# Kernel optimization log

Measured on AMD Instinct MI355X. Metric: run time of the kernel, lower is better.

Reference implementation:

```python
import jax, jax.numpy as jnp
import numpy as np

N_NODES = 50000
N_EDGES = 800000
IN_DIM = 256
HID = 64
HEADS = 4
OUT_DIM = 16
N_GRAPHS = 64
NEG_SLOPE = 0.2


def setup_inputs() -> dict:
    key = jax.random.key(0)
    ks = jax.random.split(key, 16)
    H2 = HID // 2  # conv2 out channels (heads=1, concat=False)
    H4 = HID // 4
    inp = {
        "x": jax.random.normal(ks[0], (N_NODES, IN_DIM), jnp.float32),
        "edge_index": jax.random.randint(ks[1], (2, N_EDGES), 0, N_NODES, jnp.int64),
        "batch": jnp.sort(jax.random.randint(ks[2], (N_NODES,), 0, N_GRAPHS, jnp.int64)),
        # GATConv 1: in=IN_DIM, out=HID, heads=HEADS, concat=True
        "W1": jax.random.normal(ks[3], (IN_DIM, HEADS * HID), jnp.float32) * 0.05,
        "att_src1": jax.random.normal(ks[4], (HEADS, HID), jnp.float32) * 0.1,
        "att_dst1": jax.random.normal(ks[5], (HEADS, HID), jnp.float32) * 0.1,
        "b1": jnp.zeros((HEADS * HID,), jnp.float32),
        # GATConv 2: in=HEADS*HID, out=HID/2, heads=1, concat=False
        "W2": jax.random.normal(ks[6], (HEADS * HID, H2), jnp.float32) * 0.05,
        "att_src2": jax.random.normal(ks[7], (1, H2), jnp.float32) * 0.1,
        "att_dst2": jax.random.normal(ks[8], (1, H2), jnp.float32) * 0.1,
        "b2": jnp.zeros((H2,), jnp.float32),
        "fc1_w": jax.random.normal(ks[9], (H2, H4), jnp.float32) * 0.1,
        "fc1_b": jnp.zeros((H4,), jnp.float32),
        "fc2_w": jax.random.normal(ks[10], (H4, OUT_DIM), jnp.float32) * 0.1,
        "fc2_b": jnp.zeros((OUT_DIM,), jnp.float32),
    }
    return inp


def gat_conv(x, W, att_src, att_dst, bias, src, dst, num_nodes, concat):
    """PyG-style GATConv (eval mode, self-loops already in src/dst)."""
    H, C = att_src.shape
    h = (x @ W).reshape(num_nodes, H, C)          # [N,H,C]
    a_src = (h * att_src).sum(-1)                 # [N,H]
    a_dst = (h * att_dst).sum(-1)                 # [N,H]
    e = jax.nn.leaky_relu(a_src[src] + a_dst[dst], NEG_SLOPE)  # [E,H]
    # segment softmax over destination nodes (self-loops => every segment nonempty)
    emax = jax.ops.segment_max(e, dst, num_segments=num_nodes)
    ex = jnp.exp(e - emax[dst])
    denom = jax.ops.segment_sum(ex, dst, num_segments=num_nodes)
    alpha = ex / (denom[dst] + 1e-16)             # [E,H]
    msg = h[src] * alpha[:, :, None]              # [E,H,C]
    out = jax.ops.segment_sum(msg, dst, num_segments=num_nodes)  # [N,H,C]
    out = out.reshape(num_nodes, H * C) if concat else out.mean(axis=1)
    return out + bias


def reference(x, edge_index, batch, W1, att_src1, att_dst1, b1,
              W2, att_src2, att_dst2, b2, fc1_w, fc1_b, fc2_w, fc2_b):
    num_nodes = x.shape[0]
    loops = jnp.arange(num_nodes, dtype=edge_index.dtype)
    src = jnp.concatenate([edge_index[0], loops])
    dst = jnp.concatenate([edge_index[1], loops])

    h = gat_conv(x, W1, att_src1, att_dst1, b1, src, dst, num_nodes, concat=True)
    h = jax.nn.relu(h)                                 # dropout: eval no-op
    h = gat_conv(h, W2, att_src2, att_dst2, b2, src, dst, num_nodes, concat=False)

    # global mean pool over graphs
    sums = jax.ops.segment_sum(h, batch, num_segments=N_GRAPHS)
    cnts = jax.ops.segment_sum(jnp.ones((num_nodes,), h.dtype), batch, num_segments=N_GRAPHS)
    g = sums / jnp.maximum(cnts, 1.0)[:, None]         # [G, HID/2]

    g = jax.nn.relu(g)
    g = jax.nn.relu(g @ fc1_w + fc1_b)
    g = jax.nn.relu(g @ fc2_w + fc2_b)
    return g
```

## Files before the change

kernel.cpp:

```cpp
#include <hip/hip_runtime.h>
#include <math.h>

#define NEG 0.2f
#define LMAX 1024
#define CAP 1600
#define SCHUNK 2048
typedef unsigned short u16;
typedef unsigned int u32;
typedef __bf16 bf16x8 __attribute__((ext_vector_type(8)));
typedef float f32x4 __attribute__((ext_vector_type(4)));

__device__ __forceinline__ float bf2f(u16 u) {
    union { unsigned i; float f; } x; x.i = ((unsigned)u) << 16; return x.f;
}
__device__ __forceinline__ u16 f2bf(float f) {
    union { float f; unsigned u; } x; x.f = f;
    unsigned r = x.u + 0x7fffu + ((x.u >> 16) & 1u);
    return (u16)(r >> 16);
}

__global__ void prep_all(const float* __restrict__ W1, const float* __restrict__ att_s1,
                         const float* __restrict__ att_d1, u16* __restrict__ w1x,
                         const float* __restrict__ W2, const float* __restrict__ att_s2,
                         const float* __restrict__ att_d2, u16* __restrict__ w2x,
                         int* __restrict__ bktcur, int NBK) {
    int t = threadIdx.x;
    if (blockIdx.x < 256) {
        int k = blockIdx.x;
        int c = t;
        float w = W1[k * 256 + c];
        w1x[c * 256 + k] = f2bf(w);
        int head = c >> 6;
        float vs = w * att_s1[c];
        float vd = w * att_d1[c];
#pragma unroll
        for (int mask = 1; mask < 64; mask <<= 1) {
            vs += __shfl_xor(vs, mask, 64);
            vd += __shfl_xor(vd, mask, 64);
        }
        if ((c & 63) == 0) {
            w1x[(256 + head) * 256 + k] = f2bf(vs);
            w1x[(260 + head) * 256 + k] = f2bf(vd);
            w1x[(264 + head) * 256 + k] = 0;
            w1x[(268 + head) * 256 + k] = 0;
        }
    } else {
        int k = t;
        float a_s = 0.f, a_d = 0.f;
#pragma unroll
        for (int j = 0; j < 32; ++j) {
            float w = W2[k * 32 + j];
            w2x[j * 256 + k] = f2bf(w);
            a_s += w * att_s2[j];
            a_d += w * att_d2[j];
        }
        w2x[32 * 256 + k] = f2bf(a_s);
        w2x[33 * 256 + k] = f2bf(a_d);
#pragma unroll
        for (int r = 34; r < 48; ++r) w2x[r * 256 + k] = 0;
        for (int i = t; i < NBK; i += 256) bktcur[i] = 0;
    }
}

__global__ __launch_bounds__(512) void gemm1_and_scatter(
        const float* __restrict__ x, const u16* __restrict__ w1x,
        u16* __restrict__ h1b, float* __restrict__ asad, int N,
        const int* __restrict__ ei, int* __restrict__ bktcur,
        u32* __restrict__ ebuf, int E, int ET, int NBK) {
    __shared__ __align__(16) u16 xs[2][16][264];
    __shared__ int lcnt[LMAX];
    __shared__ int lbase[LMAX];
    int t = threadIdx.x;

    if (blockIdx.x < 256) {
        int wave = t >> 6, lane = t & 63;
        int g = lane >> 4, l15 = lane & 15;

        bf16x8 wreg[3][8];
#pragma unroll
        for (int ci = 0; ci < 3; ++ci) {
            int ct = (ci == 2) ? 16 : (wave * 2 + ci);
            const u16* wp = w1x + (size_t)(ct * 16 + l15) * 256 + g * 8;
#pragma unroll
            for (int ks = 0; ks < 8; ++ks)
                wreg[ci][ks] = *reinterpret_cast<const bf16x8*>(wp + ks * 32);
        }

        int srow = t >> 5, sseg = t & 31;
        int ntiles = (N + 15) >> 4;
        int tile0 = blockIdx.x;
        if (tile0 >= ntiles) return;

        auto stage_load = [&](int tile, float4& a0, float4& a1) {
            int arow = tile * 16 + srow; if (arow > N - 1) arow = N - 1;
            const float* xp = x + (size_t)arow * 256 + sseg * 8;
            a0 = *reinterpret_cast<const float4*>(xp);
            a1 = *reinterpret_cast<const float4*>(xp + 4);
        };
        auto stage_write = [&](int buf, const float4& a0, const float4& a1) {
            uint4 o;
            o.x = (unsigned)f2bf(a0.x) | ((unsigned)f2bf(a0.y) << 16);
            o.y = (unsigned)f2bf(a0.z) | ((unsigned)f2bf(a0.w) << 16);
            o.z = (unsigned)f2bf(a1.x) | ((unsigned)f2bf(a1.y) << 16);
            o.w = (unsigned)f2bf(a1.z) | ((unsigned)f2bf(a1.w) << 16);
            *reinterpret_cast<uint4*>(&xs[buf][srow][sseg * 8]) = o;
        };

        {
            float4 a0, a1;
            stage_load(tile0, a0, a1);
            stage_write(0, a0, a1);
        }
        __syncthreads();

        int cur = 0;
        for (int tile = tile0; tile < ntiles; tile += 256) {
            int nxt = tile + 256;
            bool hasnext = nxt < ntiles;
            float4 p0, p1;
            if (hasnext) stage_load(nxt, p0, p1);

            f32x4 acc[3];
#pragma unroll
            for (int ci = 0; ci < 3; ++ci) acc[ci] = (f32x4){0.f, 0.f, 0.f, 0.f};
#pragma unroll
            for (int ks = 0; ks < 8; ++ks) {
                bf16x8 bfr = *reinterpret_cast<const bf16x8*>(&xs[cur][l15][ks * 32 + g * 8]);
#pragma unroll
                for (int ci = 0; ci < 3; ++ci)
                    acc[ci] = __builtin_amdgcn_mfma_f32_16x16x32_bf16(wreg[ci][ks], bfr, acc[ci], 0, 0, 0);
            }

            int nrow = tile * 16 + l15;
            if (nrow < N) {
#pragma unroll
                for (int ci = 0; ci < 2; ++ci) {
                    int ct = wave * 2 + ci;
                    ushort4 o;
                    o.x = f2bf(acc[ci][0]); o.y = f2bf(acc[ci][1]);
                    o.z = f2bf(acc[ci][2]); o.w = f2bf(acc[ci][3]);
                    *reinterpret_cast<ushort4*>(h1b + (size_t)nrow * 256 + ct * 16 + g * 4) = o;
                }
                if (wave == 0 && g < 2) {
#pragma unroll
                    for (int reg = 0; reg < 4; ++reg)
                        asad[(size_t)nrow * 8 + g * 4 + reg] = acc[2][reg];
                }
            }
            __syncthreads();
            if (hasnext) stage_write(cur ^ 1, p0, p1);
            __syncthreads();
            cur ^= 1;
        }
    } else {
        int cb = blockIdx.x - 256;
        for (int b = t; b < NBK; b += 512) lcnt[b] = 0;
        __syncthreads();
        int base = cb * SCHUNK;
#pragma unroll
        for (int k = 0; k < SCHUNK / 512; ++k) {
            int i = base + k * 512 + t;
            if (i < ET) {
                int d = (i < E) ? ei[E + i] : (i - E);
                atomicAdd(&lcnt[d >> 6], 1);
            }
        }
        __syncthreads();
        for (int b = t; b < NBK; b += 512) {
            int c = lcnt[b];
            lbase[b] = c ? (b * CAP + atomicAdd(&bktcur[b], c)) : 0;
        }
        __syncthreads();
        for (int b = t; b < NBK; b += 512) lcnt[b] = 0;
        __syncthreads();
#pragma unroll
        for (int k = 0; k < SCHUNK / 512; ++k) {
            int i = base + k * 512 + t;
            if (i < ET) {
                int s, d;
                if (i < E) { s = ei[i]; d = ei[E + i]; }
                else       { s = i - E; d = s; }
                int b = d >> 6;
                int idx = atomicAdd(&lcnt[b], 1);
                ebuf[lbase[b] + idx] = (u32)s | ((u32)(d & 63) << 16);
            }
        }
    }
}

__global__ __launch_bounds__(256) void bucket_csr_pad(const u32* __restrict__ ebuf,
                                                      const int* __restrict__ bktcur,
                                                      int* __restrict__ row_ptr,
                                                      int* __restrict__ rowend,
                                                      int* __restrict__ col, int N) {
    __shared__ int cnt[64];
    __shared__ int cur[64];
    int b = blockIdx.x, t = threadIdx.x;
    int v0 = b << 6;
    int s0 = b * CAP, s1 = s0 + bktcur[b];
    if (t < 64) cnt[t] = 0;
    __syncthreads();
    for (int i = s0 + t; i < s1; i += 256)
        atomicAdd(&cnt[(ebuf[i] >> 16) & 63], 1);
    __syncthreads();
    if (t < 64) {
        int c = cnt[t];
        int val = c;
#pragma unroll
        for (int off = 1; off < 64; off <<= 1) {
            int n = __shfl_up(val, off, 64);
            if (t >= off) val += n;
        }
        int excl = s0 + val - c;
        if (v0 + t < N) { row_ptr[v0 + t] = excl; rowend[v0 + t] = excl + c; }
        cur[t] = excl;
    }
    __syncthreads();
    for (int i = s0 + t; i < s1; i += 256) {
        u32 v = ebuf[i];
        int pos = atomicAdd(&cur[(v >> 16) & 63], 1);
        col[pos] = (int)(v & 0xFFFFu);
    }
}

__global__ __launch_bounds__(256) void conv1_fused(const u16* __restrict__ h1b,
                                                   const float* __restrict__ asad,
                                                   const int* __restrict__ row_ptr,
                                                   const int* __restrict__ rowend,
                                                   const int* __restrict__ col,
                                                   const float* __restrict__ b1,
                                                   u16* __restrict__ hin2b, int N) {
    __shared__ float la[4][128][4];
    __shared__ int   lc[4][128];
    int idx = blockIdx.x * blockDim.x + threadIdx.x;
    int v = idx >> 6; if (v > N - 1) v = N - 1;
    int lane = idx & 63;
    int node = threadIdx.x >> 6;
    int head = lane >> 4, l15 = lane & 15;
    float adst = asad[(size_t)v * 8 + 4 + head];
    int beg = row_ptr[v], end = rowend[v];
    int deg = end - beg;
    bool fast = (deg <= 128);
    float m = -1e30f, l = 0.f;
    if (fast) {
        float e[8]; int u[8];
#pragma unroll
        for (int i = 0; i < 8; ++i) {
            int p = beg + l15 + i * 16;
            float ev = -1e30f; int uu = 0;
            if (p < end) {
                uu = col[p];
                float tv = asad[(size_t)uu * 8 + head] + adst;
                ev = tv > 0.f ? tv : NEG * tv;
            }
            e[i] = ev; u[i] = uu;
        }
        m = e[0];
#pragma unroll
        for (int i = 1; i < 8; ++i) m = fmaxf(m, e[i]);
#pragma unroll
        for (int mask = 1; mask < 16; mask <<= 1) m = fmaxf(m, __shfl_xor(m, mask, 64));
#pragma unroll
        for (int i = 0; i < 8; ++i) {
            int j = l15 + i * 16;
            if (beg + j < end) {
                float a = __expf(e[i] - m);
                l += a;
                la[node][j][head] = a;
                if (head == 0) lc[node][j] = u[i];
            }
        }
#pragma unroll
        for (int mask = 1; mask < 16; mask <<= 1) l += __shfl_xor(l, mask, 64);
    } else {
        for (int p = beg + l15; p < end; p += 16) {
            float tv = asad[(size_t)col[p] * 8 + head] + adst;
            tv = tv > 0.f ? tv : NEG * tv;
            m = fmaxf(m, tv);
        }
#pragma unroll
        for (int mask = 1; mask < 16; mask <<= 1) m = fmaxf(m, __shfl_xor(m, mask, 64));
        for (int p = beg + l15; p < end; p += 16) {
            float tv = asad[(size_t)col[p] * 8 + head] + adst;
            tv = tv > 0.f ? tv : NEG * tv;
            l += __expf(tv - m);
        }
#pragma unroll
        for (int mask = 1; mask < 16; mask <<= 1) l += __shfl_xor(l, mask, 64);
    }
    __syncthreads();
    float inv = 1.f / (l + 1e-16f);

    float ax = 0.f, ay = 0.f, az = 0.f, aw = 0.f;
    if (fast) {
        int j = 0;
        for (; j + 3 < deg; j += 4) {
            float a0 = la[node][j + 0][head];
            float a1 = la[node][j + 1][head];
            float a2 = la[node][j + 2][head];
            float a3 = la[node][j + 3][head];
            int u0 = lc[node][j + 0], u1 = lc[node][j + 1];
            int u2 = lc[node][j + 2], u3 = lc[node][j + 3];
            ushort4 h0 = *reinterpret_cast<const ushort4*>(h1b + (size_t)u0 * 256 + lane * 4);
            ushort4 h1 = *reinterpret_cast<const ushort4*>(h1b + (size_t)u1 * 256 + lane * 4);
            ushort4 h2 = *reinterpret_cast<const ushort4*>(h1b + (size_t)u2 * 256 + lane * 4);
            ushort4 h3 = *reinterpret_cast<const ushort4*>(h1b + (size_t)u3 * 256 + lane * 4);
            ax += a0 * bf2f(h0.x) + a1 * bf2f(h1.x) + a2 * bf2f(h2.x) + a3 * bf2f(h3.x);
            ay += a0 * bf2f(h0.y) + a1 * bf2f(h1.y) + a2 * bf2f(h2.y) + a3 * bf2f(h3.y);
            az += a0 * bf2f(h0.z) + a1 * bf2f(h1.z) + a2 * bf2f(h2.z) + a3 * bf2f(h3.z);
            aw += a0 * bf2f(h0.w) + a1 * bf2f(h1.w) + a2 * bf2f(h2.w) + a3 * bf2f(h3.w);
        }
        for (; j < deg; ++j) {
            float a = la[node][j][head];
            int u = lc[node][j];
            ushort4 hv = *reinterpret_cast<const ushort4*>(h1b + (size_t)u * 256 + lane * 4);
            ax += a * bf2f(hv.x);
            ay += a * bf2f(hv.y);
            az += a * bf2f(hv.z);
            aw += a * bf2f(hv.w);
        }
    } else {
        for (int p = beg; p < end; ++p) {
            int u = col[p];
            float tv = asad[(size_t)u * 8 + head] + adst;
            tv = tv > 0.f ? tv : NEG * tv;
            float a = __expf(tv - m);
            ushort4 hv = *reinterpret_cast<const ushort4*>(h1b + (size_t)u * 256 + lane * 4);
            ax += a * bf2f(hv.x);
            ay += a * bf2f(hv.y);
            az += a * bf2f(hv.z);
            aw += a * bf2f(hv.w);
        }
    }
    int c = lane * 4;
    ushort4 o;
    o.x = f2bf(fmaxf(ax * inv + b1[c + 0], 0.f));
    o.y = f2bf(fmaxf(ay * inv + b1[c + 1], 0.f));
    o.z = f2bf(fmaxf(az * inv + b1[c + 2], 0.f));
    o.w = f2bf(fmaxf(aw * inv + b1[c + 3], 0.f));
    *reinterpret_cast<ushort4*>(hin2b + (size_t)v * 256 + c) = o;
}

__global__ __launch_bounds__(512) void gemm2_mfma(const u16* __restrict__ hin2b,
                                                  const u16* __restrict__ w2x,
                                                  u16* __restrict__ h2b,
                                                  float* __restrict__ as2,
                                                  float* __restrict__ ad2, int N) {
    __shared__ __align__(16) u16 wl[48 * 264];
    for (int f = threadIdx.x; f < 48 * 32; f += 512) {
        int r = f >> 5, cc = f & 31;
        *reinterpret_cast<uint4*>(&wl[r * 264 + cc * 8]) =
            *reinterpret_cast<const uint4*>(w2x + r * 256 + cc * 8);
    }
    __syncthreads();

    int wave = threadIdx.x >> 6, lane = threadIdx.x & 63;
    int g = lane >> 4, l15 = lane & 15;
    int ntiles = (N + 15) >> 4;
    for (int tile = blockIdx.x * 8 + wave; tile < ntiles; tile += gridDim.x * 8) {
        int r0 = tile << 4;
        int arow = r0 + l15; if (arow > N - 1) arow = N - 1;
        const u16* hp = hin2b + (size_t)arow * 256 + g * 8;

        f32x4 acc[3];
#pragma unroll
        for (int n = 0; n < 3; ++n) acc[n] = (f32x4){0.f, 0.f, 0.f, 0.f};

#pragma unroll
        for (int ks = 0; ks < 8; ++ks) {
            bf16x8 af = *reinterpret_cast<const bf16x8*>(hp + ks * 32);
#pragma unroll
            for (int n = 0; n < 3; ++n) {
                bf16x8 bf = *reinterpret_cast<const bf16x8*>(&wl[(n * 16 + l15) * 264 + ks * 32 + g * 8]);
                acc[n] = __builtin_amdgcn_mfma_f32_16x16x32_bf16(af, bf, acc[n], 0, 0, 0);
            }
        }

#pragma unroll
        for (int reg = 0; reg < 4; ++reg) {
            int grow = r0 + g * 4 + reg;
            if (grow < N) {
                h2b[(size_t)grow * 32 + l15]      = f2bf(acc[0][reg]);
                h2b[(size_t)grow * 32 + 16 + l15] = f2bf(acc[1][reg]);
                if (l15 == 0) as2[grow] = acc[2][reg];
                if (l15 == 1) ad2[grow] = acc[2][reg];
            }
        }
    }
}

__global__ __launch_bounds__(256) void conv2_fused(const u16* __restrict__ h2b,
                                                   const float* __restrict__ as2,
                                                   const float* __restrict__ ad2,
                                                   const int* __restrict__ row_ptr,
                                                   const int* __restrict__ rowend,
                                                   const int* __restrict__ col,
                                                   const float* __restrict__ b2,
                                                   float* __restrict__ out2, int N) {
    __shared__ float la[8][128];
    __shared__ int   lc[8][128];
    int idx = blockIdx.x * blockDim.x + threadIdx.x;
    int v = idx >> 5; if (v > N - 1) v = N - 1;
    int lane = idx & 31;
    int node = threadIdx.x >> 5;
    float adst = ad2[v];
    int beg = row_ptr[v], end = rowend[v];
    int deg = end - beg;
    bool fast = (deg <= 128);
    float m = -1e30f, l = 0.f;
    if (fast) {
        float e[4]; int u[4];
#pragma unroll
        for (int i = 0; i < 4; ++i) {
            int p = beg + lane + i * 32;
            float ev = -1e30f; int uu = 0;
            if (p < end) {
                uu = col[p];
                float tv = as2[uu] + adst;
                ev = tv > 0.f ? tv : NEG * tv;
            }
            e[i] = ev; u[i] = uu;
        }
        m = fmaxf(fmaxf(e[0], e[1]), fmaxf(e[2], e[3]));
#pragma unroll
        for (int mask = 1; mask < 32; mask <<= 1) m = fmaxf(m, __shfl_xor(m, mask, 64));
#pragma unroll
        for (int i = 0; i < 4; ++i) {
            int j = lane + i * 32;
            if (beg + j < end) {
                float a = __expf(e[i] - m);
                l += a;
                la[node][j] = a;
                lc[node][j] = u[i];
            }
        }
#pragma unroll
        for (int mask = 1; mask < 32; mask <<= 1) l += __shfl_xor(l, mask, 64);
    } else {
        for (int p = beg + lane; p < end; p += 32) {
            float tv = as2[col[p]] + adst;
            tv = tv > 0.f ? tv : NEG * tv;
            m = fmaxf(m, tv);
        }
#pragma unroll
        for (int mask = 1; mask < 32; mask <<= 1) m = fmaxf(m, __shfl_xor(m, mask, 64));
        for (int p = beg + lane; p < end; p += 32) {
            float tv = as2[col[p]] + adst;
            tv = tv > 0.f ? tv : NEG * tv;
            l += __expf(tv - m);
        }
#pragma unroll
        for (int mask = 1; mask < 32; mask <<= 1) l += __shfl_xor(l, mask, 64);
    }
    __syncthreads();
    float inv = 1.f / (l + 1e-16f);

    float acc = 0.f;
    if (fast) {
        int j = 0;
        for (; j + 3 < deg; j += 4) {
            float a0 = la[node][j + 0], a1 = la[node][j + 1];
            float a2 = la[node][j + 2], a3 = la[node][j + 3];
            int u0 = lc[node][j + 0], u1 = lc[node][j + 1];
            int u2 = lc[node][j + 2], u3 = lc[node][j + 3];
            acc += a0 * bf2f(h2b[(size_t)u0 * 32 + lane])
                 + a1 * bf2f(h2b[(size_t)u1 * 32 + lane])
                 + a2 * bf2f(h2b[(size_t)u2 * 32 + lane])
                 + a3 * bf2f(h2b[(size_t)u3 * 32 + lane]);
        }
        for (; j < deg; ++j)
            acc += la[node][j] * bf2f(h2b[(size_t)lc[node][j] * 32 + lane]);
    } else {
        for (int p = beg; p < end; ++p) {
            int u = col[p];
            float tv = as2[u] + adst;
            tv = tv > 0.f ? tv : NEG * tv;
            acc += __expf(tv - m) * bf2f(h2b[(size_t)u * 32 + lane]);
        }
    }
    out2[(size_t)v * 32 + lane] = acc * inv + b2[lane];
}

__global__ __launch_bounds__(256) void pool_fc(const float* __restrict__ out2,
                                               const int* __restrict__ batch,
                                               const float* __restrict__ fc1w,
                                               const float* __restrict__ fc1b,
                                               const float* __restrict__ fc2w,
                                               const float* __restrict__ fc2b,
                                               float* __restrict__ out, int N) {
    int g = blockIdx.x;
    int lo = 0, hi = N;
    while (lo < hi) { int mid = (lo + hi) >> 1; if (batch[mid] < g) lo = mid + 1; else hi = mid; }
    int s = lo;
    lo = 0; hi = N;
    while (lo < hi) { int mid = (lo + hi) >> 1; if (batch[mid] < g + 1) lo = mid + 1; else hi = mid; }
    int e = lo;

    int c = threadIdx.x & 31, grp = threadIdx.x >> 5;
    float sum = 0.f;
    for (int r = s + grp; r < e; r += 8) sum += out2[(size_t)r * 32 + c];
    __shared__ float part[8][32];
    part[grp][c] = sum;
    __syncthreads();
    __shared__ float g0[32];
    if (grp == 0) {
        float tot = 0.f;
#pragma unroll
        for (int q = 0; q < 8; ++q) tot += part[q][c];
        float cnt = (float)(e - s);
        g0[c] = fmaxf(tot / fmaxf(cnt, 1.0f), 0.f);
    }
    __syncthreads();
    __shared__ float z1[16];
    if (threadIdx.x < 16) {
        float a = fc1b[threadIdx.x];
        for (int k = 0; k < 32; ++k) a += g0[k] * fc1w[k * 16 + threadIdx.x];
        z1[threadIdx.x] = fmaxf(a, 0.f);
    }
    __syncthreads();
    if (threadIdx.x < 16) {
        float a = fc2b[threadIdx.x];
        for (int k = 0; k < 16; ++k) a += z1[k] * fc2w[k * 16 + threadIdx.x];
        out[g * 16 + threadIdx.x] = fmaxf(a, 0.f);
    }
}

extern "C" void kernel_launch(void* const* d_in, const int* in_sizes, int n_in,
                              void* d_out, int out_size, void* d_ws, size_t ws_size,
                              hipStream_t stream) {
    const float* x      = (const float*)d_in[0];
    const int*   ei     = (const int*)d_in[1];
    const int*   batch  = (const int*)d_in[2];
    const float* W1     = (const float*)d_in[3];
    const float* att_s1 = (const float*)d_in[4];
    const float* att_d1 = (const float*)d_in[5];
    const float* b1     = (const float*)d_in[6];
    const float* W2     = (const float*)d_in[7];
    const float* att_s2 = (const float*)d_in[8];
    const float* att_d2 = (const float*)d_in[9];
    const float* b2     = (const float*)d_in[10];
    const float* fc1w   = (const float*)d_in[11];
    const float* fc1b   = (const float*)d_in[12];
    const float* fc2w   = (const float*)d_in[13];
    const float* fc2b   = (const float*)d_in[14];
    float* out = (float*)d_out;

    int N = in_sizes[0] / 256;
    int E = in_sizes[1] / 2;
    int ET = E + N;
    int NBK = (N + 63) >> 6;
    int nchunks = (ET + SCHUNK - 1) / SCHUNK;

    char* ws = (char*)d_ws;
    size_t off = 0;
    auto alloc = [&](size_t bytes) { size_t o = off; off = (off + bytes + 255) & ~255ULL; return o; };
    u16*  w1x    = (u16*)(ws + alloc(272 * 256 * 2));
    u16*  w2x    = (u16*)(ws + alloc(48 * 256 * 2));
    u16*  h1b    = (u16*)(ws + alloc((size_t)N * 256 * 2));
    float* asad  = (float*)(ws + alloc((size_t)N * 8 * 4));
    u16*  hin2b  = (u16*)(ws + alloc((size_t)N * 256 * 2));
    u16*  h2b    = (u16*)(ws + alloc((size_t)N * 32 * 2));
    float* as2   = (float*)(ws + alloc((size_t)N * 4));
    float* ad2   = (float*)(ws + alloc((size_t)N * 4));
    float* out2  = (float*)(ws + alloc((size_t)N * 32 * 4));
    int* row_ptr = (int*)(ws + alloc((size_t)N * 4));
    int* rowend  = (int*)(ws + alloc((size_t)N * 4));
    int* col     = (int*)(ws + alloc((size_t)NBK * CAP * 4));
    int* bktcur  = (int*)(ws + alloc((size_t)NBK * 4));
    u32* ebuf    = (u32*)(ws + alloc((size_t)NBK * CAP * 4));
    (void)ws_size; (void)n_in; (void)out_size;

    prep_all<<<257, 256, 0, stream>>>(W1, att_s1, att_d1, w1x, W2, att_s2, att_d2, w2x, bktcur, NBK);

    gemm1_and_scatter<<<256 + nchunks, 512, 0, stream>>>(x, w1x, h1b, asad, N,
                                                         ei, bktcur, ebuf, E, ET, NBK);

    bucket_csr_pad<<<NBK, 256, 0, stream>>>(ebuf, bktcur, row_ptr, rowend, col, N);

    conv1_fused<<<(N * 64 + 255) / 256, 256, 0, stream>>>(h1b, asad, row_ptr, rowend, col, b1, hin2b, N);

    gemm2_mfma<<<256, 512, 0, stream>>>(hin2b, w2x, h2b, as2, ad2, N);
    conv2_fused<<<(N * 32 + 255) / 256, 256, 0, stream>>>(h2b, as2, ad2, row_ptr, rowend, col, b2, out2, N);

    pool_fc<<<64, 256, 0, stream>>>(out2, batch, fc1w, fc1b, fc2w, fc2b, out, N);
}
```

Baseline: 181.3 us.

## Fuse conv2 projection GEMM into conv1 aggregation epilogue via per-block MFMA

Result: slower. 191.8 us (+5.8%).

```diff
diff --git a/kernel.cpp b/kernel.cpp
--- a/kernel.cpp
+++ b/kernel.cpp
@@ -223,15 +223,19 @@
     }
 }
 
-__global__ __launch_bounds__(256) void conv1_fused(const u16* __restrict__ h1b,
-                                                   const float* __restrict__ asad,
-                                                   const int* __restrict__ row_ptr,
-                                                   const int* __restrict__ rowend,
-                                                   const int* __restrict__ col,
-                                                   const float* __restrict__ b1,
-                                                   u16* __restrict__ hin2b, int N) {
+__global__ __launch_bounds__(256) void conv1_g2(const u16* __restrict__ h1b,
+                                                const float* __restrict__ asad,
+                                                const int* __restrict__ row_ptr,
+                                                const int* __restrict__ rowend,
+                                                const int* __restrict__ col,
+                                                const float* __restrict__ b1,
+                                                const u16* __restrict__ w2x,
+                                                u16* __restrict__ h2b,
+                                                float* __restrict__ as2,
+                                                float* __restrict__ ad2, int N) {
     __shared__ float la[4][128][4];
     __shared__ int   lc[4][128];
+    __shared__ __align__(16) u16 rows[4][268];
     int idx = blockIdx.x * blockDim.x + threadIdx.x;
     int v = idx >> 6; if (v > N - 1) v = N - 1;
     int lane = idx & 63;
@@ -338,52 +342,43 @@
     o.y = f2bf(fmaxf(ay * inv + b1[c + 1], 0.f));
     o.z = f2bf(fmaxf(az * inv + b1[c + 2], 0.f));
     o.w = f2bf(fmaxf(aw * inv + b1[c + 3], 0.f));
-    *reinterpret_cast<ushort4*>(hin2b + (size_t)v * 256 + c) = o;
-}
-
-__global__ __launch_bounds__(512) void gemm2_mfma(const u16* __restrict__ hin2b,
-                                                  const u16* __restrict__ w2x,
-                                                  u16* __restrict__ h2b,
-                                                  float* __restrict__ as2,
-                                                  float* __restrict__ ad2, int N) {
-    __shared__ __align__(16) u16 wl[48 * 264];
-    for (int f = threadIdx.x; f < 48 * 32; f += 512) {
-        int r = f >> 5, cc = f & 31;
-        *reinterpret_cast<uint4*>(&wl[r * 264 + cc * 8]) =
-            *reinterpret_cast<const uint4*>(w2x + r * 256 + cc * 8);
-    }
-    __syncthreads();
-
-    int wave = threadIdx.x >> 6, lane = threadIdx.x & 63;
-    int g = lane >> 4, l15 = lane & 15;
-    int ntiles = (N + 15) >> 4;
-    for (int tile = blockIdx.x * 8 + wave; tile < ntiles; tile += gridDim.x * 8) {
-        int r0 = tile << 4;
-        int arow = r0 + l15; if (arow > N - 1) arow = N - 1;
-        const u16* hp = hin2b + (size_t)arow * 256 + g * 8;
-
-        f32x4 acc[3];
-#pragma unroll
-        for (int n = 0; n < 3; ++n) acc[n] = (f32x4){0.f, 0.f, 0.f, 0.f};
-
+    *reinterpret_cast<ushort4*>(&rows[node][lane * 4]) = o;
+    __syncthreads();
+
+    int wv = threadIdx.x >> 6;
+    if (wv < 3) {
+        int g = lane >> 4;
+        f32x4 acc = (f32x4){0.f, 0.f, 0.f, 0.f};
+        const u16* wp = w2x + (size_t)(wv * 16 + l15) * 256 + g * 8;
 #pragma unroll
         for (int ks = 0; ks < 8; ++ks) {
-            bf16x8 af = *reinterpret_cast<const bf16x8*>(hp + ks * 32);
-#pragma unroll
-            for (int n = 0; n < 3; ++n) {
-                bf16x8 bf = *reinterpret_cast<const bf16x8*>(&wl[(n * 16 + l15) * 264 + ks * 32 + g * 8]);
-                acc[n] = __builtin_amdgcn_mfma_f32_16x16x32_bf16(af, bf, acc[n], 0, 0, 0);
-            }
-        }
-
-#pragma unroll
-        for (int reg = 0; reg < 4; ++reg) {
-            int grow = r0 + g * 4 + reg;
-            if (grow < N) {
-                h2b[(size_t)grow * 32 + l15]      = f2bf(acc[0][reg]);
-                h2b[(size_t)grow * 32 + 16 + l15] = f2bf(acc[1][reg]);
-                if (l15 == 0) as2[grow] = acc[2][reg];
-                if (l15 == 1) ad2[grow] = acc[2][reg];
+            bf16x8 af = *reinterpret_cast<const bf16x8*>(&rows[l15 & 3][ks * 32 + g * 8]);
+            bf16x8 bf = *reinterpret_cast<const bf16x8*>(wp + ks * 32);
+            acc = __builtin_amdgcn_mfma_f32_16x16x32_bf16(af, bf, acc, 0, 0, 0);
+        }
+        if (g == 0) {
+            int vbase = blockIdx.x * 4;
+            if (wv < 2) {
+#pragma unroll
+                for (int reg = 0; reg < 4; ++reg) {
+                    int n = vbase + reg;
+                    if (n < N) h2b[(size_t)n * 32 + wv * 16 + l15] = f2bf(acc[reg]);
+                }
+            } else {
+                if (l15 == 0) {
+#pragma unroll
+                    for (int reg = 0; reg < 4; ++reg) {
+                        int n = vbase + reg;
+                        if (n < N) as2[n] = acc[reg];
+                    }
+                }
+                if (l15 == 1) {
+#pragma unroll
+                    for (int reg = 0; reg < 4; ++reg) {
+                        int n = vbase + reg;
+                        if (n < N) ad2[n] = acc[reg];
+                    }
+                }
             }
         }
     }
@@ -558,7 +553,6 @@
     u16*  w2x    = (u16*)(ws + alloc(48 * 256 * 2));
     u16*  h1b    = (u16*)(ws + alloc((size_t)N * 256 * 2));
     float* asad  = (float*)(ws + alloc((size_t)N * 8 * 4));
-    u16*  hin2b  = (u16*)(ws + alloc((size_t)N * 256 * 2));
     u16*  h2b    = (u16*)(ws + alloc((size_t)N * 32 * 2));
     float* as2   = (float*)(ws + alloc((size_t)N * 4));
     float* ad2   = (float*)(ws + alloc((size_t)N * 4));
@@ -577,9 +571,9 @@
 
     bucket_csr_pad<<<NBK, 256, 0, stream>>>(ebuf, bktcur, row_ptr, rowend, col, N);
 
-    conv1_fused<<<(N * 64 + 255) / 256, 256, 0, stream>>>(h1b, asad, row_ptr, rowend, col, b1, hin2b, N);
-
-    gemm2_mfma<<<256, 512, 0, stream>>>(hin2b, w2x, h2b, as2, ad2, N);
+    conv1_g2<<<(N * 64 + 255) / 256, 256, 0, stream>>>(h1b, asad, row_ptr, rowend, col, b1,
+                                                       w2x, h2b, as2, ad2, N);
+
     conv2_fused<<<(N * 32 + 255) / 256, 256, 0, stream>>>(h2b, as2, ad2, row_ptr, rowend, col, b2, out2, N);
 
     pool_fc<<<64, 256, 0, stream>>>(out2, batch, fc1w, fc1b, fc2w, fc2b, out, N);
```
